# Kernel tuning notes

Hardware: AMD Instinct MI355X
Metric: run time of the kernel (lower is better)

Reference implementation:

```python
import jax, jax.numpy as jnp
import numpy as np

VOCAB = 50257
D = 768      # d_model
E = 4        # n_experts
R = 32       # low-rank expert rank
B = 4        # batch
T = 512      # seq_len
LN_EPS = 1e-5


def setup_inputs() -> dict:
    key = jax.random.key(0)
    ks = jax.random.split(key, 8)
    n = lambda k, shape, scale: jax.random.normal(k, shape, dtype=jnp.float32) * scale
    return {
        "idx": jax.random.randint(ks[0], (B, T), 0, VOCAB),
        "W_emb": n(ks[1], (VOCAB, D), 0.02),            # tied embedding / lm head
        "G": n(ks[2], (E, D), 0.02),                     # expert gating signatures
        "W_in": n(ks[3], (E, D, R), 1.0 / np.sqrt(D)),   # per-expert input proj
        "W_rec": n(ks[4], (E, R, R), 1.0 / np.sqrt(R)),  # per-expert recurrent matrix
        "W_out": n(ks[5], (E, R, D), 1.0 / np.sqrt(R)),  # per-expert output proj
        "ln_gamma": jnp.ones((D,), dtype=jnp.float32),
        "ln_beta": jnp.zeros((D,), dtype=jnp.float32),
    }


def _layernorm(x, g, b):
    m = jnp.mean(x, axis=-1, keepdims=True)
    v = jnp.var(x, axis=-1, keepdims=True)
    return (x - m) * jax.lax.rsqrt(v + LN_EPS) * g + b


def reference(idx, W_emb, G, W_in, W_rec, W_out, ln_gamma, ln_beta):
    # idx: [B,T] int64 token ids
    x = W_emb[idx]                      # [B,T,D] embedding gather
    xT = jnp.swapaxes(x, 0, 1)          # [T,B,D] scan over time
    nE, nR = W_in.shape[0], W_in.shape[2]
    s0 = jnp.zeros((nE, idx.shape[0], nR), dtype=x.dtype)  # reset_state at t=0

    def step(states, x_t):
        # states: [E,B,R] per-expert recurrent state; x_t: [B,D]
        scores = x_t @ G.T                                         # [B,E] routing
        onehot = jax.nn.one_hot(jnp.argmax(scores, axis=-1), nE,
                                dtype=x_t.dtype)                   # [B,E] winner
        cand = jnp.tanh(jnp.einsum('bd,edr->ebr', x_t, W_in)
                        + jnp.einsum('ebr,ers->ebs', states, W_rec))  # [E,B,R]
        sel = jnp.swapaxes(onehot, 0, 1)[..., None]                # [E,B,1]
        new_states = sel * cand + (1.0 - sel) * states             # winner updates state
        y = jnp.einsum('be,ebr,erd->bd', onehot, cand, W_out) + x_t  # residual out
        return new_states, y

    _, ys = jax.lax.scan(step, s0, xT)          # ys: [T,B,D]
    h = _layernorm(jnp.swapaxes(ys, 0, 1), ln_gamma, ln_beta)  # [B,T,D]
    logits = h @ W_emb.T                         # [B,T,VOCAB] tied head
    return logits
```

## Files before the change

### kernel.cpp

```cpp
#include <hip/hip_runtime.h>
#include <hip/hip_bf16.h>
#include <stdint.h>

#define VOCAB 50257
#define NPAD  50304
#define D 768
#define E 4
#define R 32
#define B 4
#define T 512
#define NTOK (B*T)

typedef float f32x4 __attribute__((ext_vector_type(4)));
typedef short s16x8 __attribute__((ext_vector_type(8)));

__device__ __forceinline__ void async16(const void* g, void* l) {
    __builtin_amdgcn_global_load_lds(
        (const __attribute__((address_space(1))) uint32_t*)g,
        (__attribute__((address_space(3))) uint32_t*)l, 16, 0, 0);
}

__global__ __launch_bounds__(256) void k_embed_route(
    const int* __restrict__ idx, const float* __restrict__ Wemb,
    const float* __restrict__ G, const float* __restrict__ Win,
    float* __restrict__ xbuf, int* __restrict__ winner, float* __restrict__ ubuf)
{
    int tok = blockIdx.x;
    int tid = threadIdx.x;
    __shared__ float xs[D];
    __shared__ float sc[E];
    __shared__ float up[8][R];

    int token = idx[tok];
    const float* wrow = Wemb + (size_t)token * D;
    float x0 = wrow[tid], x1 = wrow[tid + 256], x2 = wrow[tid + 512];
    xs[tid] = x0; xs[tid + 256] = x1; xs[tid + 512] = x2;
    float* xg = xbuf + (size_t)tok * D;
    xg[tid] = x0; xg[tid + 256] = x1; xg[tid + 512] = x2;
    __syncthreads();

    int wave = tid >> 6, lane = tid & 63;
    {
        const float* g = G + wave * D;
        float p = 0.f;
        for (int d = lane; d < D; d += 64) p += xs[d] * g[d];
        for (int off = 32; off; off >>= 1) p += __shfl_down(p, off);
        if (lane == 0) sc[wave] = p;
    }
    __syncthreads();
    float s0 = sc[0], s1 = sc[1], s2 = sc[2], s3 = sc[3];
    int e = 0; float best = s0;
    if (s1 > best) { best = s1; e = 1; }
    if (s2 > best) { best = s2; e = 2; }
    if (s3 > best) { best = s3; e = 3; }
    if (tid == 0) winner[tok] = e;

    int r = tid & 31, chunk = tid >> 5;
    const float* wi = Win + (size_t)e * D * R;
    float p = 0.f;
    int d0 = chunk * 96;
    for (int d = d0; d < d0 + 96; ++d) p += xs[d] * wi[d * R + r];
    up[chunk][r] = p;
    __syncthreads();
    if (tid < R) {
        float s = 0.f;
        #pragma unroll
        for (int ch = 0; ch < 8; ++ch) s += up[ch][tid];
        ubuf[(size_t)tok * R + tid] = s;
    }
}

__global__ __launch_bounds__(64) void k_scan(
    const int* __restrict__ winner, const float* __restrict__ ubuf,
    const float* __restrict__ Wrec, float* __restrict__ cbuf)
{
    int b = blockIdx.x >> 2;
    int e = blockIdx.x & 3;
    int j = threadIdx.x;
    __shared__ float s_lds[R];
    __shared__ int   tlist[T];

    const int* wb = winner + b * T;

    unsigned long long lanemask_lt = (j == 0) ? 0ull : (~0ull >> (64 - j));
    int base = 0;
    for (int rr = 0; rr < T / 64; ++rr) {
        int t = rr * 64 + j;
        bool match = (wb[t] == e);
        unsigned long long m = __ballot(match);
        if (match) tlist[base + __popcll(m & lanemask_lt)] = t;
        base += __popcll(m);
    }
    int total = base;

    float wr[R];
    if (j < R) {
        s_lds[j] = 0.f;
        #pragma unroll
        for (int i = 0; i < R; ++i) wr[i] = Wrec[(size_t)e * R * R + i * R + j];
    }
    __syncthreads();
    if (j >= R) return;

    const float* ub = ubuf + (size_t)b * T * R;
    float*       cb = cbuf + (size_t)b * T * R;

    int   t0 = 0, t1 = 0;
    float u0 = 0.f, u1 = 0.f;
    if (total > 0) { t0 = tlist[0]; u0 = ub[t0 * R + j]; }
    if (total > 1) { t1 = tlist[1]; u1 = ub[t1 * R + j]; }

    for (int k = 0; k < total; ++k) {
        int t = t0; float uj = u0;
        t0 = t1; u0 = u1;
        if (k + 2 < total) { int t2 = tlist[k + 2]; t1 = t2; u1 = ub[t2 * R + j]; }

        float a0 = uj, a1 = 0.f, a2 = 0.f, a3 = 0.f;
        #pragma unroll
        for (int q = 0; q < 8; ++q) {
            float4 sv = *(const float4*)&s_lds[q * 4];
            a0 += sv.x * wr[q * 4 + 0]; a1 += sv.y * wr[q * 4 + 1];
            a2 += sv.z * wr[q * 4 + 2]; a3 += sv.w * wr[q * 4 + 3];
        }
        float acc = (a0 + a1) + (a2 + a3);
        float ex = __expf(2.f * acc);
        float th = 1.f - 2.f * __builtin_amdgcn_rcpf(ex + 1.f);
        cb[t * R + j] = th;
        s_lds[j] = th;
    }
}

__global__ __launch_bounds__(256) void k_out_ln(
    const float* __restrict__ xbuf, const int* __restrict__ winner,
    const float* __restrict__ cbuf, const float* __restrict__ Wout,
    const float* __restrict__ gamma, const float* __restrict__ beta,
    __hip_bfloat16* __restrict__ hbuf)
{
    int tok = blockIdx.x, tid = threadIdx.x;
    __shared__ float cs[R];
    __shared__ float w1[4], w2[4];
    int e = winner[tok];
    if (tid < R) cs[tid] = cbuf[(size_t)tok * R + tid];
    __syncthreads();

    const float* wo = Wout + (size_t)e * R * D;
    const float* xg = xbuf + (size_t)tok * D;
    float y[3];
    #pragma unroll
    for (int kk = 0; kk < 3; ++kk) {
        int d = tid + kk * 256;
        float acc = xg[d];
        #pragma unroll
        for (int r = 0; r < R; ++r) acc += cs[r] * wo[r * D + d];
        y[kk] = acc;
    }
    float s1 = y[0] + y[1] + y[2];
    float s2 = y[0] * y[0] + y[1] * y[1] + y[2] * y[2];
    int wave = tid >> 6, lane = tid & 63;
    for (int off = 32; off; off >>= 1) { s1 += __shfl_down(s1, off); s2 += __shfl_down(s2, off); }
    if (lane == 0) { w1[wave] = s1; w2[wave] = s2; }
    __syncthreads();
    float m = (w1[0] + w1[1] + w1[2] + w1[3]) * (1.f / D);
    float v = (w2[0] + w2[1] + w2[2] + w2[3]) * (1.f / D) - m * m;
    float rstd = rsqrtf(v + 1e-5f);
    #pragma unroll
    for (int kk = 0; kk < 3; ++kk) {
        int d = tid + kk * 256;
        float hn = (y[kk] - m) * rstd * gamma[d] + beta[d];
        hbuf[(size_t)tok * D + d] = __float2bfloat16(hn);
    }
}

__global__ __launch_bounds__(256) void k_cvt(
    const float* __restrict__ Wemb, __hip_bfloat16* __restrict__ Wb)
{
    long i = (long)(blockIdx.x * 256 + threadIdx.x) * 4;
    const long total = (long)NPAD * D;
    const long valid = (long)VOCAB * D;
    if (i >= total) return;
    float4 v;
    if (i < valid) v = *(const float4*)(Wemb + i);
    else           v = make_float4(0.f, 0.f, 0.f, 0.f);
    union { ushort4 u4; __hip_bfloat16 h[4]; } pk;
    pk.h[0] = __float2bfloat16(v.x); pk.h[1] = __float2bfloat16(v.y);
    pk.h[2] = __float2bfloat16(v.z); pk.h[3] = __float2bfloat16(v.w);
    *(ushort4*)((unsigned short*)Wb + i) = pk.u4;
}

#define BM 128
#define BN 128
#define BK 64
#define NWG (16 * 393)
__global__ __launch_bounds__(256) void k_gemm(
    const __hip_bfloat16* __restrict__ A,
    const __hip_bfloat16* __restrict__ Bm,
    float* __restrict__ Cmat)
{
    __shared__ __align__(16) char lds[BM * BK * 2 + BN * BK * 2];
    const int tid = threadIdx.x;
    const int orig = blockIdx.x;
    const int wg = (orig & 7) * (NWG / 8) + (orig >> 3);
    const int m0 = (wg & 15) * BM;
    const int n0 = (wg >> 4) * BN;
    const int wave = tid >> 6, lane = tid & 63;
    const int wm = (wave >> 1) * 64, wn = (wave & 1) * 64;
    const int l15 = lane & 15, quad = lane >> 4;

    f32x4 acc[4][4] = {};

    const int srow = tid >> 3;
    const int skel = (tid & 7) * 8;
    const size_t aBase = (size_t)(m0 + srow) * 768 + skel;
    const size_t bBase = (size_t)(n0 + srow) * 768 + skel;
    char* aT = lds;
    char* bT = lds + BM * BK * 2;
    const int ldsOff = tid * 16;

    for (int k0 = 0; k0 < 768; k0 += BK) {
        #pragma unroll
        for (int rr = 0; rr < 4; ++rr) {
            async16(A  + aBase + (size_t)rr * 32 * 768 + k0, aT + rr * 4096 + ldsOff);
            async16(Bm + bBase + (size_t)rr * 32 * 768 + k0, bT + rr * 4096 + ldsOff);
        }
        __syncthreads();
        #pragma unroll
        for (int kk = 0; kk < BK; kk += 32) {
            s16x8 af[4], bf[4];
            #pragma unroll
            for (int i = 0; i < 4; ++i)
                af[i] = *(const s16x8*)(aT + ((wm + i * 16 + l15) * BK + kk + quad * 8) * 2);
            #pragma unroll
            for (int j = 0; j < 4; ++j)
                bf[j] = *(const s16x8*)(bT + ((wn + j * 16 + l15) * BK + kk + quad * 8) * 2);
            #pragma unroll
            for (int i = 0; i < 4; ++i)
                #pragma unroll
                for (int j = 0; j < 4; ++j)
                    acc[i][j] = __builtin_amdgcn_mfma_f32_16x16x32_bf16(af[i], bf[j], acc[i][j], 0, 0, 0);
        }
        __syncthreads();
    }

    #pragma unroll
    for (int i = 0; i < 4; ++i) {
        #pragma unroll
        for (int j = 0; j < 4; ++j) {
            int col = n0 + wn + j * 16 + l15;
            if (col < VOCAB) {
                #pragma unroll
                for (int r = 0; r < 4; ++r) {
                    int row = m0 + wm + i * 16 + quad * 4 + r;
                    Cmat[(size_t)row * VOCAB + col] = acc[i][j][r];
                }
            }
        }
    }
}

extern "C" void kernel_launch(void* const* d_in, const int* in_sizes, int n_in,
                              void* d_out, int out_size, void* d_ws, size_t ws_size,
                              hipStream_t stream)
{
    const int*   idx   = (const int*)d_in[0];
    const float* Wemb  = (const float*)d_in[1];
    const float* G     = (const float*)d_in[2];
    const float* Win   = (const float*)d_in[3];
    const float* Wrec  = (const float*)d_in[4];
    const float* Wout  = (const float*)d_in[5];
    const float* gamma = (const float*)d_in[6];
    const float* beta  = (const float*)d_in[7];
    float* out = (float*)d_out;

    char* ws = (char*)d_ws;
    float*          xbuf   = (float*)(ws);
    int*            winner = (int*)  (ws + 6291456);
    float*          ubuf   = (float*)(ws + 6299648);
    float*          cbuf   = (float*)(ws + 6561792);
    __hip_bfloat16* hbuf   = (__hip_bfloat16*)(ws + 6823936);
    __hip_bfloat16* wembb  = (__hip_bfloat16*)(ws + 9969664);

    k_cvt<<<(NPAD * D / 4 + 255) / 256, 256, 0, stream>>>(Wemb, wembb);
    k_embed_route<<<NTOK, 256, 0, stream>>>(idx, Wemb, G, Win, xbuf, winner, ubuf);
    k_scan<<<B * E, 64, 0, stream>>>(winner, ubuf, Wrec, cbuf);
    k_out_ln<<<NTOK, 256, 0, stream>>>(xbuf, winner, cbuf, Wout, gamma, beta, hbuf);
    k_gemm<<<NWG, 256, 0, stream>>>(hbuf, wembb, out);
}
```

Baseline: 878.4 us.

## Rewrite LM-head GEMM with 256x256 tiles, double-buffered LDS and swizzle

Rebuilds the tied-head GEMM around 256x256 tiles computed by 512 threads, with a double-buffered 128KB LDS pipeline. The next K slice is prefetched through async global-to-LDS loads, interleaved with MFMA phases and waited on with explicit vmcnt counts. LDS addresses get an XOR swizzle to cut bank conflicts, and s_setprio is raised around the MFMA bursts. Vocab padding grows to a multiple of 256, so the bf16 weight copy and the wasted columns get larger. The large LDS footprint also limits how many workgroups fit on a CU.

```diff
diff --git a/kernel.cpp b/kernel.cpp
--- a/kernel.cpp
+++ b/kernel.cpp
@@ -3,7 +3,7 @@
 #include <stdint.h>
 
 #define VOCAB 50257
-#define NPAD  50304
+#define NPAD  50432
 #define D 768
 #define E 4
 #define R 32
@@ -187,62 +187,124 @@
     *(ushort4*)((unsigned short*)Wb + i) = pk.u4;
 }
 
-#define BM 128
-#define BN 128
+#define BM 256
+#define BN 256
 #define BK 64
-#define NWG (16 * 393)
-__global__ __launch_bounds__(256) void k_gemm(
+#define MB (NTOK / BM)
+#define NB (NPAD / BN)
+#define NWG (MB * NB)
+__global__ __launch_bounds__(512, 2) void k_gemm(
     const __hip_bfloat16* __restrict__ A,
     const __hip_bfloat16* __restrict__ Bm,
     float* __restrict__ Cmat)
 {
-    __shared__ __align__(16) char lds[BM * BK * 2 + BN * BK * 2];
+    __shared__ __align__(16) char lds[131072];
     const int tid = threadIdx.x;
     const int orig = blockIdx.x;
     const int wg = (orig & 7) * (NWG / 8) + (orig >> 3);
-    const int m0 = (wg & 15) * BM;
-    const int n0 = (wg >> 4) * BN;
+    const int m0 = (wg & (MB - 1)) * BM;
+    const int n0 = (wg / MB) * BN;
     const int wave = tid >> 6, lane = tid & 63;
-    const int wm = (wave >> 1) * 64, wn = (wave & 1) * 64;
+    const int wm = (wave & 1) * 128;
+    const int wn = (wave >> 1) * 64;
     const int l15 = lane & 15, quad = lane >> 4;
 
-    f32x4 acc[4][4] = {};
-
-    const int srow = tid >> 3;
-    const int skel = (tid & 7) * 8;
-    const size_t aBase = (size_t)(m0 + srow) * 768 + skel;
-    const size_t bBase = (size_t)(n0 + srow) * 768 + skel;
-    char* aT = lds;
-    char* bT = lds + BM * BK * 2;
-    const int ldsOff = tid * 16;
-
-    for (int k0 = 0; k0 < 768; k0 += BK) {
-        #pragma unroll
-        for (int rr = 0; rr < 4; ++rr) {
-            async16(A  + aBase + (size_t)rr * 32 * 768 + k0, aT + rr * 4096 + ldsOff);
-            async16(Bm + bBase + (size_t)rr * 32 * 768 + k0, bT + rr * 4096 + ldsOff);
-        }
-        __syncthreads();
-        #pragma unroll
-        for (int kk = 0; kk < BK; kk += 32) {
-            s16x8 af[4], bf[4];
-            #pragma unroll
-            for (int i = 0; i < 4; ++i)
-                af[i] = *(const s16x8*)(aT + ((wm + i * 16 + l15) * BK + kk + quad * 8) * 2);
-            #pragma unroll
-            for (int j = 0; j < 4; ++j)
-                bf[j] = *(const s16x8*)(bT + ((wn + j * 16 + l15) * BK + kk + quad * 8) * 2);
-            #pragma unroll
-            for (int i = 0; i < 4; ++i)
-                #pragma unroll
-                for (int j = 0; j < 4; ++j)
-                    acc[i][j] = __builtin_amdgcn_mfma_f32_16x16x32_bf16(af[i], bf[j], acc[i][j], 0, 0, 0);
-        }
-        __syncthreads();
+    f32x4 acc[8][4] = {};
+
+    const int srowS = tid >> 2;
+    const int skelS = (((tid & 3) ^ ((tid >> 2) & 3)) * 8);
+    const size_t aBase = (size_t)(m0 + srowS) * 768 + skelS;
+    const size_t bBase = (size_t)(n0 + srowS) * 768 + skelS;
+    const int ldsPos = tid * 16;
+
+    auto stageA = [&](char* buf, int kg, int h) {
+        async16(A + aBase + kg + h * 32,                      buf + h * 16384 + ldsPos);
+        async16(A + aBase + (size_t)128 * 768 + kg + h * 32,  buf + h * 16384 + 8192 + ldsPos);
+    };
+    auto stageB = [&](char* buf, int kg, int h) {
+        async16(Bm + bBase + kg + h * 32,                     buf + 32768 + h * 16384 + ldsPos);
+        async16(Bm + bBase + (size_t)128 * 768 + kg + h * 32, buf + 32768 + h * 16384 + 8192 + ldsPos);
+    };
+
+    const int swz = ((quad ^ (l15 & 3)) << 4);
+
+    stageA(lds, 0, 0); stageB(lds, 0, 0); stageA(lds, 0, 1); stageB(lds, 0, 1);
+
+    for (int t = 0; t < 12; ++t) {
+        char* bufC = lds + (t & 1) * 65536;
+        char* bufN = lds + ((t + 1) & 1) * 65536;
+        const int k1 = (t + 1) * BK;
+        const bool pre = (t < 11);
+        s16x8 af[8], bfr[2];
+
+        asm volatile("s_waitcnt vmcnt(4)" ::: "memory");
+        __builtin_amdgcn_s_barrier();
+        __builtin_amdgcn_sched_barrier(0);
+        if (pre) stageA(bufN, k1, 0);
+        #pragma unroll
+        for (int i = 0; i < 8; ++i)
+            af[i] = *(const s16x8*)(bufC + (wm + i * 16 + l15) * 64 + swz);
+        #pragma unroll
+        for (int j = 0; j < 2; ++j)
+            bfr[j] = *(const s16x8*)(bufC + 32768 + (wn + j * 16 + l15) * 64 + swz);
+        __builtin_amdgcn_s_setprio(1);
+        #pragma unroll
+        for (int i = 0; i < 8; ++i) {
+            acc[i][0] = __builtin_amdgcn_mfma_f32_16x16x32_bf16(af[i], bfr[0], acc[i][0], 0, 0, 0);
+            acc[i][1] = __builtin_amdgcn_mfma_f32_16x16x32_bf16(af[i], bfr[1], acc[i][1], 0, 0, 0);
+        }
+        __builtin_amdgcn_s_setprio(0);
+
+        __builtin_amdgcn_s_barrier();
+        __builtin_amdgcn_sched_barrier(0);
+        if (pre) stageB(bufN, k1, 0);
+        #pragma unroll
+        for (int j = 0; j < 2; ++j)
+            bfr[j] = *(const s16x8*)(bufC + 32768 + (wn + (j + 2) * 16 + l15) * 64 + swz);
+        __builtin_amdgcn_s_setprio(1);
+        #pragma unroll
+        for (int i = 0; i < 8; ++i) {
+            acc[i][2] = __builtin_amdgcn_mfma_f32_16x16x32_bf16(af[i], bfr[0], acc[i][2], 0, 0, 0);
+            acc[i][3] = __builtin_amdgcn_mfma_f32_16x16x32_bf16(af[i], bfr[1], acc[i][3], 0, 0, 0);
+        }
+        __builtin_amdgcn_s_setprio(0);
+
+        if (t == 11) asm volatile("s_waitcnt vmcnt(0)" ::: "memory");
+        else         asm volatile("s_waitcnt vmcnt(4)" ::: "memory");
+        __builtin_amdgcn_s_barrier();
+        __builtin_amdgcn_sched_barrier(0);
+        if (pre) stageA(bufN, k1, 1);
+        #pragma unroll
+        for (int i = 0; i < 8; ++i)
+            af[i] = *(const s16x8*)(bufC + 16384 + (wm + i * 16 + l15) * 64 + swz);
+        #pragma unroll
+        for (int j = 0; j < 2; ++j)
+            bfr[j] = *(const s16x8*)(bufC + 49152 + (wn + j * 16 + l15) * 64 + swz);
+        __builtin_amdgcn_s_setprio(1);
+        #pragma unroll
+        for (int i = 0; i < 8; ++i) {
+            acc[i][0] = __builtin_amdgcn_mfma_f32_16x16x32_bf16(af[i], bfr[0], acc[i][0], 0, 0, 0);
+            acc[i][1] = __builtin_amdgcn_mfma_f32_16x16x32_bf16(af[i], bfr[1], acc[i][1], 0, 0, 0);
+        }
+        __builtin_amdgcn_s_setprio(0);
+
+        __builtin_amdgcn_s_barrier();
+        __builtin_amdgcn_sched_barrier(0);
+        if (pre) stageB(bufN, k1, 1);
+        #pragma unroll
+        for (int j = 0; j < 2; ++j)
+            bfr[j] = *(const s16x8*)(bufC + 49152 + (wn + (j + 2) * 16 + l15) * 64 + swz);
+        __builtin_amdgcn_s_setprio(1);
+        #pragma unroll
+        for (int i = 0; i < 8; ++i) {
+            acc[i][2] = __builtin_amdgcn_mfma_f32_16x16x32_bf16(af[i], bfr[0], acc[i][2], 0, 0, 0);
+            acc[i][3] = __builtin_amdgcn_mfma_f32_16x16x32_bf16(af[i], bfr[1], acc[i][3], 0, 0, 0);
+        }
+        __builtin_amdgcn_s_setprio(0);
     }
 
     #pragma unroll
-    for (int i = 0; i < 4; ++i) {
+    for (int i = 0; i < 8; ++i) {
         #pragma unroll
         for (int j = 0; j < 4; ++j) {
             int col = n0 + wn + j * 16 + l15;
@@ -283,5 +345,5 @@
     k_embed_route<<<NTOK, 256, 0, stream>>>(idx, Wemb, G, Win, xbuf, winner, ubuf);
     k_scan<<<B * E, 64, 0, stream>>>(winner, ubuf, Wrec, cbuf);
     k_out_ln<<<NTOK, 256, 0, stream>>>(xbuf, winner, cbuf, Wout, gamma, beta, hbuf);
-    k_gemm<<<NWG, 256, 0, stream>>>(hbuf, wembb, out);
-}
+    k_gemm<<<NWG, 512, 0, stream>>>(hbuf, wembb, out);
+}
```

New measurement: 789.0 us. -10.2%, faster.
